# Kernel tuning notes

Hardware: AMD Instinct MI355X
Metric: run time of the kernel (lower is better)

Reference implementation:

```python
import jax, jax.numpy as jnp
import numpy as np

N = 50000      # nodes
E = 800000     # edges per relation (avg degree 16)
D = 128        # in_feat == out_feat
H = 4          # num_heads
DH = D // H    # head dim = 32
NEG_SLOPE = 0.2  # DGL GATConv default


def setup_inputs() -> dict:
    key = jax.random.key(0)
    ks = jax.random.split(key, 12)
    inp = {
        "x": jax.random.normal(ks[0], (N, D), jnp.float32),
        "W_r0": jax.random.normal(ks[1], (D, D), jnp.float32) * (1.0 / np.sqrt(D)),
        "attn_l_r0": jax.random.normal(ks[2], (H, DH), jnp.float32),
        "attn_r_r0": jax.random.normal(ks[3], (H, DH), jnp.float32),
        "W_r1": jax.random.normal(ks[4], (D, D), jnp.float32) * (1.0 / np.sqrt(D)),
        "attn_l_r1": jax.random.normal(ks[5], (H, DH), jnp.float32),
        "attn_r_r1": jax.random.normal(ks[6], (H, DH), jnp.float32),
        "loop_weight": jax.random.normal(ks[7], (D, D), jnp.float32) * (1.0 / np.sqrt(D)),
        "h_bias": jnp.zeros((D,), jnp.float32),
        "src_r0": jax.random.randint(ks[8], (E,), 0, N, jnp.int32),
        "dst_r0": jax.random.randint(ks[9], (E,), 0, N, jnp.int32),
        "src_r1": jax.random.randint(ks[10], (E,), 0, N, jnp.int32),
        "dst_r1": jax.random.randint(ks[11], (E,), 0, N, jnp.int32),
    }
    return inp


def _gat_conv(x, W, attn_l, attn_r, src, dst):
    """One DGL-style GATConv (no bias, no conv activation). Returns [N,H,DH]."""
    feat = (x @ W).reshape(N, H, DH)                 # projected features
    el = jnp.einsum('nhd,hd->nh', feat, attn_l)      # [N,H] attn on source
    er = jnp.einsum('nhd,hd->nh', feat, attn_r)      # [N,H] attn on dest
    e = jax.nn.leaky_relu(el[src] + er[dst], NEG_SLOPE)  # [E,H]
    # edge softmax over incoming edges of each dst node (stable)
    emax = jax.ops.segment_max(e, dst, num_segments=N)   # [N,H]
    ex = jnp.exp(e - emax[dst])                          # [E,H]
    denom = jax.ops.segment_sum(ex, dst, num_segments=N) # [N,H]
    alpha = ex / denom[dst]                              # [E,H]
    msg = feat[src] * alpha[:, :, None]                  # [E,H,DH]
    return jax.ops.segment_sum(msg, dst, num_segments=N) # [N,H,DH]


def reference(x, W_r0, attn_l_r0, attn_r_r0, W_r1, attn_l_r1, attn_r_r1,
              loop_weight, h_bias, src_r0, dst_r0, src_r1, dst_r1):
    # HeteroGraphConv with default 'sum' cross-relation aggregation
    h = _gat_conv(x, W_r0, attn_l_r0, attn_r_r0, src_r0, dst_r0) \
      + _gat_conv(x, W_r1, attn_l_r1, attn_r_r1, src_r1, dst_r1)
    h = h.reshape(N, H * DH)          # flatten heads -> [N, out_feat]
    h = h + x @ loop_weight           # self loop
    h = h + h_bias                    # bias
    h = jax.nn.relu(h)                # activation (dropout=0, no norm, no FFN)
    return h
```

## Files before the change

kernel.cpp:

```cpp
#include <hip/hip_runtime.h>
#include <hip/hip_bf16.h>

#define NN 50000
#define EE 800000
#define DD 128
#define HH 4
#define NEG_SLOPE 0.2f

#define BSH 9
#define NBUCK 98
#define CH 8192
#define NBLK 98
#define NSEG (2 * NBUCK * NBLK)

typedef __attribute__((ext_vector_type(8))) short bf16x8;
typedef __attribute__((ext_vector_type(4))) float f32x4;
typedef __attribute__((ext_vector_type(8))) unsigned short ushrt8;

static __device__ __forceinline__ float bf2f(ushort u) {
    union { unsigned int ui; float f; } v; v.ui = ((unsigned int)u) << 16; return v.f;
}
static __device__ __forceinline__ void split1(float v, ushort& h, ushort& l) {
    __hip_bfloat16 hb = __float2bfloat16(v);
    float hf = __bfloat162float(hb);
    __hip_bfloat16 lb = __float2bfloat16(v - hf);
    h = *(ushort*)&hb; l = *(ushort*)&lb;
}

#define XB 6250
#define WB 192
__global__ __launch_bounds__(256) void prep_kernel(
    const float* __restrict__ x,
    const float* __restrict__ W0, const float* __restrict__ W1,
    const float* __restrict__ Wl,
    const int* __restrict__ dst0, const int* __restrict__ dst1,
    ushort* __restrict__ xh, ushort* __restrict__ xl, ushort* __restrict__ wt,
    int* __restrict__ hist)
{
    const int b = blockIdx.x;
    const int t = threadIdx.x;
    if (b < XB) {
        int i = b * 256 + t;
        float4 v = ((const float4*)x)[i];
        ushort4 h, l;
        split1(v.x, h.x, l.x); split1(v.y, h.y, l.y);
        split1(v.z, h.z, l.z); split1(v.w, h.w, l.w);
        *(ushort4*)&xh[(size_t)i * 4] = h;
        *(ushort4*)&xl[(size_t)i * 4] = l;
    } else if (b < XB + WB) {
        int idx = (b - XB) * 256 + t;
        int m = idx >> 14, e = idx & 16383;
        const float* W = (m == 0) ? W0 : (m == 1) ? W1 : Wl;
        int k = e >> 7, n = e & 127;
        ushort h, l; split1(W[e], h, l);
        int q = m * 4 + (k >> 5);
        int kin8 = (k >> 3) & 3, ke = k & 7;
        int sw = n & 7;
        size_t base = (size_t)q * 8192 + n * 64;
        wt[base + (((0 | kin8) ^ sw) << 3) + ke] = h;
        wt[base + (((4 | kin8) ^ sw) << 3) + ke] = l;
    } else {
        __shared__ int cnt[NBUCK];
        int hb = b - XB - WB;
        int rel = hb >= NBLK;
        int ci = hb - rel * NBLK;
        const int* __restrict__ dstA = rel ? dst1 : dst0;
        if (t < NBUCK) cnt[t] = 0;
        __syncthreads();
        int lo = ci * CH, hi = min(lo + CH, EE);
        for (int i = lo + t; i < hi; i += 256)
            atomicAdd(&cnt[dstA[i] >> BSH], 1);
        __syncthreads();
        if (t < NBUCK)
            hist[((rel * NBUCK) + t) * NBLK + ci] = cnt[t];
    }
}

__global__ __launch_bounds__(256) void scan_kernel(
    const int* __restrict__ hist, int* __restrict__ base)
{
    __shared__ int wq[4];
    const int t = threadIdx.x;
    const int lane = t & 63, wv = t >> 6;
    const int st = t * 76;
    const int en = min(st + 76, NSEG);
    int sum = 0;
    for (int i = st; i < en; ++i) sum += hist[i];
    int incl = sum;
    #pragma unroll
    for (int off = 1; off < 64; off <<= 1) {
        int u = __shfl_up(incl, off);
        if (lane >= off) incl += u;
    }
    if (lane == 63) wq[wv] = incl;
    __syncthreads();
    int woff = 0;
    #pragma unroll
    for (int w = 0; w < 4; ++w) woff += (w < wv) ? wq[w] : 0;
    int run = woff + incl - sum;
    for (int i = st; i < en; ++i) { base[i] = run; run += hist[i]; }
}

__global__ __launch_bounds__(256) void bucket_kernel(
    const int* __restrict__ src0, const int* __restrict__ dst0,
    const int* __restrict__ src1, const int* __restrict__ dst1,
    const int* __restrict__ base, unsigned int* __restrict__ pk)
{
    __shared__ int cnt[NBUCK];
    __shared__ int bs[NBUCK];
    const int hb = blockIdx.x;
    const int t = threadIdx.x;
    const int rel = hb >= NBLK;
    const int ci = hb - rel * NBLK;
    const int* __restrict__ srcA = rel ? src1 : src0;
    const int* __restrict__ dstA = rel ? dst1 : dst0;
    if (t < NBUCK) {
        cnt[t] = 0;
        bs[t] = base[((rel * NBUCK) + t) * NBLK + ci];
    }
    __syncthreads();
    int lo = ci * CH, hi = min(lo + CH, EE);
    for (int i = lo + t; i < hi; i += 256) {
        int dd = dstA[i], ss = srcA[i];
        int bk = dd >> BSH;
        int rk = atomicAdd(&cnt[bk], 1);
        pk[bs[bk] + rk] = (unsigned int)ss | ((unsigned int)(dd & 511) << 17);
    }
}

__global__ __launch_bounds__(256) void sort_kernel(
    const unsigned int* __restrict__ pk, const int* __restrict__ base,
    int* __restrict__ row0, int* __restrict__ row1, int* __restrict__ list)
{
    __shared__ int cnt[512];
    __shared__ int offs[512];
    __shared__ int wq[4];
    const int hb = blockIdx.x;
    const int t = threadIdx.x;
    const int lane = t & 63, wv = t >> 6;
    const int rel = hb >= NBUCK;
    const int bk = hb - rel * NBUCK;

    const int fs = base[((rel * NBUCK) + bk) * NBLK];
    const int fe = (rel == 1 && bk == NBUCK - 1) ? 2 * EE
                 : base[((rel * NBUCK) + bk + 1) * NBLK];

    cnt[t] = 0; cnt[t + 256] = 0;
    __syncthreads();
    for (int i = fs + t; i < fe; i += 256)
        atomicAdd(&cnt[pk[i] >> 17], 1);
    __syncthreads();

    int a = cnt[2 * t], bvl = cnt[2 * t + 1];
    int ps = a + bvl;
    int incl = ps;
    #pragma unroll
    for (int off = 1; off < 64; off <<= 1) {
        int u = __shfl_up(incl, off);
        if (lane >= off) incl += u;
    }
    if (lane == 63) wq[wv] = incl;
    __syncthreads();
    int woff = 0;
    #pragma unroll
    for (int w = 0; w < 4; ++w) woff += (w < wv) ? wq[w] : 0;
    int excl = woff + incl - ps;
    offs[2 * t] = excl;
    offs[2 * t + 1] = excl + a;
    __syncthreads();

    int* __restrict__ row = rel ? row1 : row0;
    const int fsLocal = fs - (rel ? EE : 0);
    const int d0 = bk << BSH;
    for (int j = t; j < 512; j += 256) {
        int d = d0 + j;
        if (d < NN) row[d] = fsLocal + offs[j] + cnt[j];
    }
    __syncthreads();

    for (int i = fs + t; i < fe; i += 256) {
        unsigned int u = pk[i];
        int ld = u >> 17;
        int p = atomicAdd(&offs[ld], 1);
        list[fs + p] = (int)(u & 0x1FFFF);
    }
}

__global__ __launch_bounds__(256) void proj_kernel(
    const ushort* __restrict__ xh, const ushort* __restrict__ xl,
    const ushort* __restrict__ wt,
    const float* __restrict__ al0, const float* __restrict__ ar0,
    const float* __restrict__ al1, const float* __restrict__ ar1,
    const float* __restrict__ bias,
    ushort* __restrict__ fb0, ushort* __restrict__ fb1,
    float* __restrict__ el0, float* __restrict__ er0,
    float* __restrict__ el1, float* __restrict__ er1,
    float* __restrict__ out)
{
    __shared__ ushort lds[2][8192];
    const int t = threadIdx.x;
    const int lane = t & 63, wave = t >> 6;
    const int l15 = lane & 15, lg = lane >> 4;
    const int rb = blockIdx.x * 128 + wave * 32;

    int ra0 = rb + l15;      if (ra0 > NN - 1) ra0 = NN - 1;
    int ra1 = rb + 16 + l15; if (ra1 > NN - 1) ra1 = NN - 1;
    const int kb = lg * 8;

    bf16x8 Ah0[4], Av0[4], Ah1[4], Av1[4];
    #pragma unroll
    for (int kc = 0; kc < 4; ++kc) {
        Ah0[kc] = *(const bf16x8*)&xh[(size_t)ra0 * DD + kc * 32 + kb];
        Av0[kc] = *(const bf16x8*)&xl[(size_t)ra0 * DD + kc * 32 + kb];
        Ah1[kc] = *(const bf16x8*)&xh[(size_t)ra1 * DD + kc * 32 + kb];
        Av1[kc] = *(const bf16x8*)&xl[(size_t)ra1 * DD + kc * 32 + kb];
    }

    {
        const bf16x8* g = (const bf16x8*)wt;
        bf16x8* L = (bf16x8*)lds[0];
        #pragma unroll
        for (int i = 0; i < 4; ++i) L[t + i * 256] = g[t + i * 256];
    }

    for (int m = 0; m < 3; ++m) {
        f32x4 acc0[8], acc1[8];
        #pragma unroll
        for (int nt = 0; nt < 8; ++nt) {
            acc0[nt] = (f32x4){0.f, 0.f, 0.f, 0.f};
            acc1[nt] = (f32x4){0.f, 0.f, 0.f, 0.f};
        }

        #pragma unroll
        for (int kc = 0; kc < 4; ++kc) {
            const int q = m * 4 + kc;
            __syncthreads();
            bf16x8 st0, st1, st2, st3;
            const bool hasNext = (q < 11);
            if (hasNext) {
                const bf16x8* g = (const bf16x8*)(wt + (size_t)(q + 1) * 8192);
                st0 = g[t]; st1 = g[t + 256]; st2 = g[t + 512]; st3 = g[t + 768];
            }
            const ushort* __restrict__ L = lds[kc & 1];
            #pragma unroll
            for (int nt = 0; nt < 8; ++nt) {
                const int n = nt * 16 + l15;
                const int sw = n & 7;
                bf16x8 bh = *(const bf16x8*)&L[n * 64 + (((0 | lg) ^ sw) << 3)];
                bf16x8 bv = *(const bf16x8*)&L[n * 64 + (((4 | lg) ^ sw) << 3)];
                acc0[nt] = __builtin_amdgcn_mfma_f32_16x16x32_bf16(Ah0[kc], bh, acc0[nt], 0, 0, 0);
                acc0[nt] = __builtin_amdgcn_mfma_f32_16x16x32_bf16(Ah0[kc], bv, acc0[nt], 0, 0, 0);
                acc0[nt] = __builtin_amdgcn_mfma_f32_16x16x32_bf16(Av0[kc], bh, acc0[nt], 0, 0, 0);
                acc1[nt] = __builtin_amdgcn_mfma_f32_16x16x32_bf16(Ah1[kc], bh, acc1[nt], 0, 0, 0);
                acc1[nt] = __builtin_amdgcn_mfma_f32_16x16x32_bf16(Ah1[kc], bv, acc1[nt], 0, 0, 0);
                acc1[nt] = __builtin_amdgcn_mfma_f32_16x16x32_bf16(Av1[kc], bh, acc1[nt], 0, 0, 0);
            }
            if (hasNext) {
                bf16x8* Lw = (bf16x8*)lds[(kc & 1) ^ 1];
                Lw[t] = st0; Lw[t + 256] = st1; Lw[t + 512] = st2; Lw[t + 768] = st3;
            }
        }

        if (m < 2) {
            ushort* __restrict__ fb = m ? fb1 : fb0;
            const float* __restrict__ alm = m ? al1 : al0;
            const float* __restrict__ arm = m ? ar1 : ar0;
            float* __restrict__ elm = m ? el1 : el0;
            float* __restrict__ erm = m ? er1 : er0;
            #pragma unroll
            for (int tt = 0; tt < 2; ++tt) {
                float pl[4][4], pr[4][4];
                #pragma unroll
                for (int r = 0; r < 4; ++r)
                    #pragma unroll
                    for (int h = 0; h < 4; ++h) { pl[r][h] = 0.f; pr[r][h] = 0.f; }
                #pragma unroll
                for (int nt = 0; nt < 8; ++nt) {
                    const int col = nt * 16 + l15;
                    const float wlv = alm[col], wrv = arm[col];
                    #pragma unroll
                    for (int r = 0; r < 4; ++r) {
                        const float v = tt ? acc1[nt][r] : acc0[nt][r];
                        pl[r][nt >> 1] += v * wlv;
                        pr[r][nt >> 1] += v * wrv;
                        const int row = rb + tt * 16 + lg * 4 + r;
                        if (row < NN) {
                            __hip_bfloat16 hb = __float2bfloat16(v);
                            fb[(size_t)row * DD + col] = *(ushort*)&hb;
                        }
                    }
                }
                #pragma unroll
                for (int msk = 1; msk < 16; msk <<= 1)
                    #pragma unroll
                    for (int r = 0; r < 4; ++r)
                        #pragma unroll
                        for (int h = 0; h < 4; ++h) {
                            pl[r][h] += __shfl_xor(pl[r][h], msk);
                            pr[r][h] += __shfl_xor(pr[r][h], msk);
                        }
                if (l15 < 4) {
                    #pragma unroll
                    for (int r = 0; r < 4; ++r) {
                        const int row = rb + tt * 16 + lg * 4 + r;
                        if (row < NN) {
                            const float plv = l15 == 0 ? pl[r][0] : l15 == 1 ? pl[r][1]
                                            : l15 == 2 ? pl[r][2] : pl[r][3];
                            const float prv = l15 == 0 ? pr[r][0] : l15 == 1 ? pr[r][1]
                                            : l15 == 2 ? pr[r][2] : pr[r][3];
                            elm[(size_t)row * 4 + l15] = plv;
                            erm[(size_t)row * 4 + l15] = prv;
                        }
                    }
                }
            }
        } else {
            #pragma unroll
            for (int tt = 0; tt < 2; ++tt)
                #pragma unroll
                for (int nt = 0; nt < 8; ++nt) {
                    const int col = nt * 16 + l15;
                    const float bv = bias[col];
                    #pragma unroll
                    for (int r = 0; r < 4; ++r) {
                        const int row = rb + tt * 16 + lg * 4 + r;
                        const float v = tt ? acc1[nt][r] : acc0[nt][r];
                        if (row < NN) out[(size_t)row * DD + col] = v + bv;
                    }
                }
        }
    }
}

__global__ __launch_bounds__(256) void agg_kernel(
    const int* __restrict__ row0, const int* __restrict__ list0,
    const float* __restrict__ el0, const float* __restrict__ er0,
    const int* __restrict__ row1, const int* __restrict__ list1,
    const float* __restrict__ el1, const float* __restrict__ er1,
    const ushort* __restrict__ fb0, const ushort* __restrict__ fb1,
    float* __restrict__ out)
{
    const int d = blockIdx.x * 4 + (threadIdx.x >> 6);
    const int lane = threadIdx.x & 63;
    if (d >= NN) return;
    const int g = lane >> 4;
    const int l16 = lane & 15;
    const int c = l16 * 8;
    const int h = l16 >> 2;

    float tot[8] = {0.f, 0.f, 0.f, 0.f, 0.f, 0.f, 0.f, 0.f};

    #pragma unroll
    for (int rel = 0; rel < 2; ++rel) {
        const int* __restrict__ rowA = rel ? row1 : row0;
        const int* __restrict__ lst  = rel ? list1 : list0;
        const float* __restrict__ elA = rel ? el1 : el0;
        const float* __restrict__ erA = rel ? er1 : er0;
        const ushort* __restrict__ fbA = rel ? fb1 : fb0;

        const int s0 = d ? rowA[d - 1] : 0, e0 = rowA[d];
        const float erh = erA[(size_t)d * 4 + h];
        float acc[8] = {0.f, 0.f, 0.f, 0.f, 0.f, 0.f, 0.f, 0.f};
        float den = 0.f;
        for (int i = s0 + g; i < e0; i += 4) {
            int s = lst[i];
            float ev = elA[(size_t)s * 4 + h] + erh;
            ev = ev > 0.f ? ev : NEG_SLOPE * ev;
            float w = __expf(ev);
            den += w;
            ushrt8 f = *(const ushrt8*)&fbA[(size_t)s * DD + c];
            #pragma unroll
            for (int q = 0; q < 8; ++q) acc[q] += w * bf2f(f[q]);
        }
        den += __shfl_xor(den, 16); den += __shfl_xor(den, 32);
        #pragma unroll
        for (int q = 0; q < 8; ++q) {
            acc[q] += __shfl_xor(acc[q], 16);
            acc[q] += __shfl_xor(acc[q], 32);
        }
        if (e0 > s0) {
            float inv = 1.f / den;
            #pragma unroll
            for (int q = 0; q < 8; ++q) tot[q] += acc[q] * inv;
        }
    }

    if (g == 0) {
        float4 o1 = *(float4*)&out[(size_t)d * DD + c];
        float4 o2 = *(float4*)&out[(size_t)d * DD + c + 4];
        o1.x = fmaxf(o1.x + tot[0], 0.f); o1.y = fmaxf(o1.y + tot[1], 0.f);
        o1.z = fmaxf(o1.z + tot[2], 0.f); o1.w = fmaxf(o1.w + tot[3], 0.f);
        o2.x = fmaxf(o2.x + tot[4], 0.f); o2.y = fmaxf(o2.y + tot[5], 0.f);
        o2.z = fmaxf(o2.z + tot[6], 0.f); o2.w = fmaxf(o2.w + tot[7], 0.f);
        *(float4*)&out[(size_t)d * DD + c] = o1;
        *(float4*)&out[(size_t)d * DD + c + 4] = o2;
    }
}

extern "C" void kernel_launch(void* const* d_in, const int* in_sizes, int n_in,
                              void* d_out, int out_size, void* d_ws, size_t ws_size,
                              hipStream_t stream)
{
    const float* x    = (const float*)d_in[0];
    const float* W0   = (const float*)d_in[1];
    const float* al0  = (const float*)d_in[2];
    const float* ar0  = (const float*)d_in[3];
    const float* W1   = (const float*)d_in[4];
    const float* al1  = (const float*)d_in[5];
    const float* ar1  = (const float*)d_in[6];
    const float* Wl   = (const float*)d_in[7];
    const float* bias = (const float*)d_in[8];
    const int* src0   = (const int*)d_in[9];
    const int* dst0   = (const int*)d_in[10];
    const int* src1   = (const int*)d_in[11];
    const int* dst1   = (const int*)d_in[12];
    float* out = (float*)d_out;

    ushort* wsu = (ushort*)d_ws;
    ushort* xh  = wsu;
    ushort* xl  = xh + (size_t)NN * DD;
    ushort* fb0 = xl + (size_t)NN * DD;
    ushort* fb1 = fb0 + (size_t)NN * DD;
    ushort* wt  = fb1 + (size_t)NN * DD;
    float* fbase = (float*)(wt + 12 * 8192);
    float* el0  = fbase;
    float* er0  = el0 + (size_t)NN * HH;
    float* el1  = er0 + (size_t)NN * HH;
    float* er1  = el1 + (size_t)NN * HH;
    int* hist   = (int*)(er1 + (size_t)NN * HH);
    int* base   = hist + NSEG;
    int* row0   = base + NSEG;
    int* row1   = row0 + NN;
    unsigned int* pk = (unsigned int*)(row1 + NN);
    int* list   = (int*)(pk + (size_t)2 * EE);
    int* list0  = list;
    int* list1  = list + EE;

    prep_kernel<<<dim3(XB + WB + 2 * NBLK), dim3(256), 0, stream>>>(
        x, W0, W1, Wl, dst0, dst1, xh, xl, wt, hist);

    scan_kernel<<<dim3(1), dim3(256), 0, stream>>>(hist, base);

    bucket_kernel<<<dim3(2 * NBLK), dim3(256), 0, stream>>>(
        src0, dst0, src1, dst1, base, pk);

    sort_kernel<<<dim3(2 * NBUCK), dim3(256), 0, stream>>>(
        pk, base, row0, row1, list);

    proj_kernel<<<dim3((NN + 127) / 128), dim3(256), 0, stream>>>(
        xh, xl, wt, al0, ar0, al1, ar1, bias,
        fb0, fb1, el0, er0, el1, er1, out);

    agg_kernel<<<dim3((NN + 3) / 4), dim3(256), 0, stream>>>(
        row0, list0, el0, er0, row1, list1, el1, er1, fb0, fb1, out);
}
```

Before: 223.8 us.

## Merge edge bucketing into projection kernel and prefetch neighbor rows in aggregation

Edge bucketing and the bf16 projection GEMM are now one launch, with the first blocks bucketing edges and the rest projecting node rows. The two independent stages can then share the GPU concurrently and one launch gap goes away. The aggregation loop is software-pipelined: it loads the next neighbor's index, attention logit and feature row before using the current one, to hide gather latency. The merged kernel carries the projection's register and LDS footprint into the bucket blocks, and the prefetch raises register pressure in the aggregation kernel.

After: 217.2 us. -3.0%, faster.

```diff
diff --git a/kernel.cpp b/kernel.cpp
--- a/kernel.cpp
+++ b/kernel.cpp
@@ -12,6 +12,8 @@
 #define CH 8192
 #define NBLK 98
 #define NSEG (2 * NBUCK * NBLK)
+#define BKB (2 * NBLK)
+#define PJB ((NN + 127) / 128)
 
 typedef __attribute__((ext_vector_type(8))) short bf16x8;
 typedef __attribute__((ext_vector_type(4))) float f32x4;
@@ -101,92 +103,10 @@
     for (int i = st; i < en; ++i) { base[i] = run; run += hist[i]; }
 }
 
-__global__ __launch_bounds__(256) void bucket_kernel(
+__global__ __launch_bounds__(256) void projbucket_kernel(
     const int* __restrict__ src0, const int* __restrict__ dst0,
     const int* __restrict__ src1, const int* __restrict__ dst1,
-    const int* __restrict__ base, unsigned int* __restrict__ pk)
-{
-    __shared__ int cnt[NBUCK];
-    __shared__ int bs[NBUCK];
-    const int hb = blockIdx.x;
-    const int t = threadIdx.x;
-    const int rel = hb >= NBLK;
-    const int ci = hb - rel * NBLK;
-    const int* __restrict__ srcA = rel ? src1 : src0;
-    const int* __restrict__ dstA = rel ? dst1 : dst0;
-    if (t < NBUCK) {
-        cnt[t] = 0;
-        bs[t] = base[((rel * NBUCK) + t) * NBLK + ci];
-    }
-    __syncthreads();
-    int lo = ci * CH, hi = min(lo + CH, EE);
-    for (int i = lo + t; i < hi; i += 256) {
-        int dd = dstA[i], ss = srcA[i];
-        int bk = dd >> BSH;
-        int rk = atomicAdd(&cnt[bk], 1);
-        pk[bs[bk] + rk] = (unsigned int)ss | ((unsigned int)(dd & 511) << 17);
-    }
-}
-
-__global__ __launch_bounds__(256) void sort_kernel(
-    const unsigned int* __restrict__ pk, const int* __restrict__ base,
-    int* __restrict__ row0, int* __restrict__ row1, int* __restrict__ list)
-{
-    __shared__ int cnt[512];
-    __shared__ int offs[512];
-    __shared__ int wq[4];
-    const int hb = blockIdx.x;
-    const int t = threadIdx.x;
-    const int lane = t & 63, wv = t >> 6;
-    const int rel = hb >= NBUCK;
-    const int bk = hb - rel * NBUCK;
-
-    const int fs = base[((rel * NBUCK) + bk) * NBLK];
-    const int fe = (rel == 1 && bk == NBUCK - 1) ? 2 * EE
-                 : base[((rel * NBUCK) + bk + 1) * NBLK];
-
-    cnt[t] = 0; cnt[t + 256] = 0;
-    __syncthreads();
-    for (int i = fs + t; i < fe; i += 256)
-        atomicAdd(&cnt[pk[i] >> 17], 1);
-    __syncthreads();
-
-    int a = cnt[2 * t], bvl = cnt[2 * t + 1];
-    int ps = a + bvl;
-    int incl = ps;
-    #pragma unroll
-    for (int off = 1; off < 64; off <<= 1) {
-        int u = __shfl_up(incl, off);
-        if (lane >= off) incl += u;
-    }
-    if (lane == 63) wq[wv] = incl;
-    __syncthreads();
-    int woff = 0;
-    #pragma unroll
-    for (int w = 0; w < 4; ++w) woff += (w < wv) ? wq[w] : 0;
-    int excl = woff + incl - ps;
-    offs[2 * t] = excl;
-    offs[2 * t + 1] = excl + a;
-    __syncthreads();
-
-    int* __restrict__ row = rel ? row1 : row0;
-    const int fsLocal = fs - (rel ? EE : 0);
-    const int d0 = bk << BSH;
-    for (int j = t; j < 512; j += 256) {
-        int d = d0 + j;
-        if (d < NN) row[d] = fsLocal + offs[j] + cnt[j];
-    }
-    __syncthreads();
-
-    for (int i = fs + t; i < fe; i += 256) {
-        unsigned int u = pk[i];
-        int ld = u >> 17;
-        int p = atomicAdd(&offs[ld], 1);
-        list[fs + p] = (int)(u & 0x1FFFF);
-    }
-}
-
-__global__ __launch_bounds__(256) void proj_kernel(
+    const int* __restrict__ base, unsigned int* __restrict__ pk,
     const ushort* __restrict__ xh, const ushort* __restrict__ xl,
     const ushort* __restrict__ wt,
     const float* __restrict__ al0, const float* __restrict__ ar0,
@@ -199,9 +119,34 @@
 {
     __shared__ ushort lds[2][8192];
     const int t = threadIdx.x;
+
+    if (blockIdx.x < BKB) {
+        int* cnt = (int*)&lds[0][0];
+        int* bs  = cnt + 128;
+        const int hb = blockIdx.x;
+        const int rel = hb >= NBLK;
+        const int ci = hb - rel * NBLK;
+        const int* __restrict__ srcA = rel ? src1 : src0;
+        const int* __restrict__ dstA = rel ? dst1 : dst0;
+        if (t < NBUCK) {
+            cnt[t] = 0;
+            bs[t] = base[((rel * NBUCK) + t) * NBLK + ci];
+        }
+        __syncthreads();
+        int lo = ci * CH, hi = min(lo + CH, EE);
+        for (int i = lo + t; i < hi; i += 256) {
+            int dd = dstA[i], ss = srcA[i];
+            int bk = dd >> BSH;
+            int rk = atomicAdd(&cnt[bk], 1);
+            pk[bs[bk] + rk] = (unsigned int)ss | ((unsigned int)(dd & 511) << 17);
+        }
+        return;
+    }
+
+    const int pb = blockIdx.x - BKB;
     const int lane = t & 63, wave = t >> 6;
     const int l15 = lane & 15, lg = lane >> 4;
-    const int rb = blockIdx.x * 128 + wave * 32;
+    const int rb = pb * 128 + wave * 32;
 
     int ra0 = rb + l15;      if (ra0 > NN - 1) ra0 = NN - 1;
     int ra1 = rb + 16 + l15; if (ra1 > NN - 1) ra1 = NN - 1;
@@ -332,6 +277,64 @@
     }
 }
 
+__global__ __launch_bounds__(256) void sort_kernel(
+    const unsigned int* __restrict__ pk, const int* __restrict__ base,
+    int* __restrict__ row0, int* __restrict__ row1, int* __restrict__ list)
+{
+    __shared__ int cnt[512];
+    __shared__ int offs[512];
+    __shared__ int wq[4];
+    const int hb = blockIdx.x;
+    const int t = threadIdx.x;
+    const int lane = t & 63, wv = t >> 6;
+    const int rel = hb >= NBUCK;
+    const int bk = hb - rel * NBUCK;
+
+    const int fs = base[((rel * NBUCK) + bk) * NBLK];
+    const int fe = (rel == 1 && bk == NBUCK - 1) ? 2 * EE
+                 : base[((rel * NBUCK) + bk + 1) * NBLK];
+
+    cnt[t] = 0; cnt[t + 256] = 0;
+    __syncthreads();
+    for (int i = fs + t; i < fe; i += 256)
+        atomicAdd(&cnt[pk[i] >> 17], 1);
+    __syncthreads();
+
+    int a = cnt[2 * t], bvl = cnt[2 * t + 1];
+    int ps = a + bvl;
+    int incl = ps;
+    #pragma unroll
+    for (int off = 1; off < 64; off <<= 1) {
+        int u = __shfl_up(incl, off);
+        if (lane >= off) incl += u;
+    }
+    if (lane == 63) wq[wv] = incl;
+    __syncthreads();
+    int woff = 0;
+    #pragma unroll
+    for (int w = 0; w < 4; ++w) woff += (w < wv) ? wq[w] : 0;
+    int excl = woff + incl - ps;
+    offs[2 * t] = excl;
+    offs[2 * t + 1] = excl + a;
+    __syncthreads();
+
+    int* __restrict__ row = rel ? row1 : row0;
+    const int fsLocal = fs - (rel ? EE : 0);
+    const int d0 = bk << BSH;
+    for (int j = t; j < 512; j += 256) {
+        int d = d0 + j;
+        if (d < NN) row[d] = fsLocal + offs[j] + cnt[j];
+    }
+    __syncthreads();
+
+    for (int i = fs + t; i < fe; i += 256) {
+        unsigned int u = pk[i];
+        int ld = u >> 17;
+        int p = atomicAdd(&offs[ld], 1);
+        list[fs + p] = (int)(u & 0x1FFFF);
+    }
+}
+
 __global__ __launch_bounds__(256) void agg_kernel(
     const int* __restrict__ row0, const int* __restrict__ list0,
     const float* __restrict__ el0, const float* __restrict__ er0,
@@ -362,16 +365,33 @@
         const float erh = erA[(size_t)d * 4 + h];
         float acc[8] = {0.f, 0.f, 0.f, 0.f, 0.f, 0.f, 0.f, 0.f};
         float den = 0.f;
-        for (int i = s0 + g; i < e0; i += 4) {
+
+        int i = s0 + g;
+        float elvA = 0.f;
+        ushrt8 fA = (ushrt8){0, 0, 0, 0, 0, 0, 0, 0};
+        if (i < e0) {
             int s = lst[i];
-            float ev = elA[(size_t)s * 4 + h] + erh;
+            elvA = elA[(size_t)s * 4 + h];
+            fA = *(const ushrt8*)&fbA[(size_t)s * DD + c];
+        }
+        while (i < e0) {
+            const int inext = i + 4;
+            float elvB = 0.f;
+            ushrt8 fB = (ushrt8){0, 0, 0, 0, 0, 0, 0, 0};
+            if (inext < e0) {
+                int s = lst[inext];
+                elvB = elA[(size_t)s * 4 + h];
+                fB = *(const ushrt8*)&fbA[(size_t)s * DD + c];
+            }
+            float ev = elvA + erh;
             ev = ev > 0.f ? ev : NEG_SLOPE * ev;
             float w = __expf(ev);
             den += w;
-            ushrt8 f = *(const ushrt8*)&fbA[(size_t)s * DD + c];
             #pragma unroll
-            for (int q = 0; q < 8; ++q) acc[q] += w * bf2f(f[q]);
-        }
+            for (int q = 0; q < 8; ++q) acc[q] += w * bf2f(fA[q]);
+            i = inext; elvA = elvB; fA = fB;
+        }
+
         den += __shfl_xor(den, 16); den += __shfl_xor(den, 32);
         #pragma unroll
         for (int q = 0; q < 8; ++q) {
@@ -441,16 +461,14 @@
 
     scan_kernel<<<dim3(1), dim3(256), 0, stream>>>(hist, base);
 
-    bucket_kernel<<<dim3(2 * NBLK), dim3(256), 0, stream>>>(
-        src0, dst0, src1, dst1, base, pk);
+    projbucket_kernel<<<dim3(BKB + PJB), dim3(256), 0, stream>>>(
+        src0, dst0, src1, dst1, base, pk,
+        xh, xl, wt, al0, ar0, al1, ar1, bias,
+        fb0, fb1, el0, er0, el1, er1, out);
 
     sort_kernel<<<dim3(2 * NBUCK), dim3(256), 0, stream>>>(
         pk, base, row0, row1, list);
 
-    proj_kernel<<<dim3((NN + 127) / 128), dim3(256), 0, stream>>>(
-        xh, xl, wt, al0, ar0, al1, ar1, bias,
-        fb0, fb1, el0, er0, el1, er1, out);
-
     agg_kernel<<<dim3((NN + 3) / 4), dim3(256), 0, stream>>>(
         row0, list0, el0, er0, row1, list1, el1, er1, fb0, fb1, out);
 }
```
